# Kernel optimization log

Hardware: AMD Instinct MI355X
Metric: run time of the kernel (lower is better)

The kernel has to match this reference:

```python
import jax, jax.numpy as jnp
import numpy as np

B, N, D, L = 32, 1024, 128, 2  # batch graphs, nodes, hidden dim, num GIN layers
BN_EPS = 1e-5


def _batchnorm(x2d, gamma, beta):
    # Training-mode BatchNorm1d over flattened (B*N, D) with biased variance
    mean = jnp.mean(x2d, axis=0)
    var = jnp.mean(jnp.square(x2d - mean), axis=0)
    return (x2d - mean) * (gamma / jnp.sqrt(var + BN_EPS)) + beta


def setup_inputs() -> dict:
    key = jax.random.key(0)
    ks = jax.random.split(key, 12)
    s = 1.0 / np.sqrt(D)  # torch Linear default init scale
    inp = {
        "x": jax.random.normal(ks[0], (B, N, D), dtype=jnp.float32),
        "padded_nei": jax.random.randint(ks[1], (B, N, 8), 0, N, dtype=jnp.int64),
        "adj": jax.random.uniform(ks[2], (B, N, N), dtype=jnp.float32),
        # stacked per-layer params [L, ...]
        "W1": jax.random.uniform(ks[3], (L, D, D), jnp.float32, -s, s),
        "b1": jax.random.uniform(ks[4], (L, D), jnp.float32, -s, s),
        "W2": jax.random.uniform(ks[5], (L, D, D), jnp.float32, -s, s),
        "b2": jax.random.uniform(ks[6], (L, D), jnp.float32, -s, s),
        "g_in": jnp.ones((L, D), jnp.float32),   # MLP-internal BN gamma
        "be_in": jnp.zeros((L, D), jnp.float32),  # MLP-internal BN beta
        "g_out": jnp.ones((L, D), jnp.float32),  # GraphCNN outer BN gamma
        "be_out": jnp.zeros((L, D), jnp.float32),
    }
    return inp


def reference(x, padded_nei, adj, W1, b1, W2, b2, g_in, be_in, g_out, be_out):
    h = x  # [B, N, D]
    for l in range(L):
        # sum-pooling over neighbors via batched dense adjacency matmul
        pooled = jnp.einsum('bij,bjd->bid', adj, h)  # [B, N, D]
        # MLP: Linear -> BN -> ReLU -> Linear
        z = pooled @ W1[l] + b1[l]
        z = jax.nn.relu(_batchnorm(z.reshape(-1, D), g_in[l], be_in[l])).reshape(B, N, D)
        z = z @ W2[l] + b2[l]
        # outer BatchNorm1d + ReLU
        h = jax.nn.relu(_batchnorm(z.reshape(-1, D), g_out[l], be_out[l])).reshape(B, N, D)
    return h
```

## Files before the change

### kernel.cpp

```cpp
#include <hip/hip_runtime.h>
#include <stdint.h>


#define BB 32
#define NN 1024
#define DD 128
#define RR 32768

typedef __bf16 bf16_t;
typedef bf16_t bf16x8 __attribute__((ext_vector_type(8)));
typedef unsigned short us8 __attribute__((ext_vector_type(8)));
typedef float f32x4 __attribute__((ext_vector_type(4)));

__device__ __forceinline__ unsigned short f2b(float f) {
  unsigned u = __float_as_uint(f);
  u += 0x7fff + ((u >> 16) & 1);
  return (unsigned short)(u >> 16);
}
__device__ __forceinline__ float b2f(unsigned short s) {
  return __uint_as_float((unsigned)s << 16);
}

#define GLL(GP, LP)                                              \
  __builtin_amdgcn_global_load_lds(                              \
      (const __attribute__((address_space(1))) void*)(GP),       \
      (__attribute__((address_space(3))) void*)(LP), 16, 0, 0)

__global__ __launch_bounds__(256) void k0_prep(const float* __restrict__ x,
                                               const float* __restrict__ adj,
                                               const float* __restrict__ W1,
                                               const float* __restrict__ W2,
                                               unsigned short* __restrict__ hT,
                                               unsigned short* __restrict__ W1T,
                                               unsigned short* __restrict__ W2T,
                                               unsigned short* __restrict__ adjB) {
  const int tid = threadIdx.x;
  if (blockIdx.x >= 512) {
    size_t i8 = ((size_t)(blockIdx.x - 512) * 256 + tid) * 8;
    float4 a = *(const float4*)(adj + i8);
    float4 b = *(const float4*)(adj + i8 + 4);
    alignas(16) unsigned short t[8] = {f2b(a.x), f2b(a.y), f2b(a.z), f2b(a.w),
                                       f2b(b.x), f2b(b.y), f2b(b.z), f2b(b.w)};
    *(uint4*)(adjB + i8) = *(const uint4*)t;
    return;
  }
  if (blockIdx.x < 256) {
    const int b = blockIdx.x >> 3, nt = blockIdx.x & 7;
    __shared__ alignas(16) unsigned short T[128][136];
    const int r = tid >> 1, c0 = (tid & 1) * 64;
    const float* src = x + ((size_t)(b * 8 + nt) * 128 + r) * 128 + c0;
#pragma unroll
    for (int i = 0; i < 64; i += 4) {
      float4 v = *(const float4*)(src + i);
      int c = c0 + i;
      T[c][r] = f2b(v.x); T[c + 1][r] = f2b(v.y);
      T[c + 2][r] = f2b(v.z); T[c + 3][r] = f2b(v.w);
    }
    __syncthreads();
    const int d = tid >> 1, n0 = (tid & 1) * 64;
    unsigned short* dst = hT + ((size_t)b * DD + d) * NN + nt * 128 + n0;
#pragma unroll
    for (int i = 0; i < 64; i += 8)
      *(uint4*)(dst + i) = *(const uint4*)&T[d][n0 + i];
  } else {
    int idx = (blockIdx.x - 256) * 256 + tid;
    int w = idx >> 15;
    int rem = idx & 32767;
    int l = rem >> 14;
    int n = (rem >> 7) & 127;
    int k = rem & 127;
    const float* W = w ? W2 : W1;
    unsigned short* WT = w ? W2T : W1T;
    WT[((size_t)l * 128 + n) * 128 + k] = f2b(W[((size_t)l * 128 + k) * 128 + n]);
  }
}

__global__ __launch_bounds__(256, 2) void kA_pool_lin(
    const unsigned short* __restrict__ adjB, const unsigned short* __restrict__ hT,
    const unsigned short* __restrict__ WT, const float* __restrict__ bias,
    unsigned short* __restrict__ z1b, float* __restrict__ gsum,
    float* __restrict__ gsq) {
  const int mt = blockIdx.x, b = blockIdx.y;
  const int tid = threadIdx.x;
  const int wave = tid >> 6, lane = tid & 63;
  const int wc = wave * 32;
  const int ln = lane & 15, q = lane >> 4;

  __shared__ union {
    struct {
      unsigned short A[3][4096];
      unsigned short B[3][8192];
    } s;
    unsigned short As2[64][136];
  } sm;

  bf16x8 wfr[4][2];
#pragma unroll
  for (int ks = 0; ks < 4; ks++)
#pragma unroll
    for (int j = 0; j < 2; j++)
      wfr[ks][j] = *(const bf16x8*)&WT[(size_t)(wc + j * 16 + ln) * 128 + ks * 32 + q * 8];
  asm volatile("s_waitcnt vmcnt(0)" ::: "memory");

  const unsigned short* adjb = adjB + ((size_t)b * NN + mt * 64) * NN;
  const unsigned short* hTb = hT + (size_t)b * DD * NN;

  const int srow = tid >> 3;
  const int sseg = (((tid & 7) ^ (srow & 7)) << 3);
  const unsigned short* gA = adjb + (size_t)srow * NN + sseg;
  const unsigned short* gB = hTb + (size_t)srow * NN + sseg;

#define STAGE(P, K0)                                \
  do {                                              \
    unsigned short* ap = sm.s.A[(P)];               \
    unsigned short* bp = sm.s.B[(P)];               \
    GLL(gA + (K0), ap + tid * 8);                   \
    GLL(gA + 32 * NN + (K0), ap + 2048 + tid * 8);  \
    GLL(gB + (K0), bp + tid * 8);                   \
    GLL(gB + 32 * NN + (K0), bp + 2048 + tid * 8);  \
    GLL(gB + 64 * NN + (K0), bp + 4096 + tid * 8);  \
    GLL(gB + 96 * NN + (K0), bp + 6144 + tid * 8);  \
  } while (0)

  STAGE(0, 0);
  STAGE(1, 64);
  STAGE(2, 128);

  f32x4 acc1[4][2];
  f32x4 zero = {0.f, 0.f, 0.f, 0.f};
#pragma unroll
  for (int i = 0; i < 4; i++) { acc1[i][0] = zero; acc1[i][1] = zero; }

  const int xorv = (ln & 7) << 4;

#pragma unroll
  for (int t = 0; t < 16; ++t) {
    const int p = t % 3;
    if (t < 14)
      asm volatile("s_waitcnt vmcnt(12)" ::: "memory");
    else if (t == 14)
      asm volatile("s_waitcnt vmcnt(6)" ::: "memory");
    else
      asm volatile("s_waitcnt vmcnt(0)" ::: "memory");
    __builtin_amdgcn_s_barrier();
    __builtin_amdgcn_sched_barrier(0);
    {
      const char* Ab = (const char*)sm.s.A[p];
      const char* Bb = (const char*)sm.s.B[p];
#pragma unroll
      for (int kk = 0; kk < 2; kk++) {
        const int co = ((kk << 6) + (q << 4)) ^ xorv;
        bf16x8 af[4], bfr[2];
#pragma unroll
        for (int i = 0; i < 4; i++)
          af[i] = *(const bf16x8*)(Ab + (i * 16 + ln) * 128 + co);
#pragma unroll
        for (int j = 0; j < 2; j++)
          bfr[j] = *(const bf16x8*)(Bb + (wc + j * 16 + ln) * 128 + co);
#pragma unroll
        for (int i = 0; i < 4; i++)
#pragma unroll
          for (int j = 0; j < 2; j++)
            acc1[i][j] = __builtin_amdgcn_mfma_f32_16x16x32_bf16(af[i], bfr[j], acc1[i][j], 0, 0, 0);
      }
    }
    __builtin_amdgcn_sched_barrier(0);
    __builtin_amdgcn_s_barrier();
    __builtin_amdgcn_sched_barrier(0);
    if (t < 13) STAGE(p, (t + 3) * 64);
  }
#undef STAGE

#pragma unroll
  for (int i = 0; i < 4; i++) {
    int row = i * 16 + q * 4;
#pragma unroll
    for (int j = 0; j < 2; j++) {
      int col = wc + j * 16 + ln;
#pragma unroll
      for (int r = 0; r < 4; r++) sm.As2[row + r][col] = f2b(acc1[i][j][r]);
    }
  }
  __syncthreads();

  f32x4 acc2[4][2];
#pragma unroll
  for (int i = 0; i < 4; i++) { acc2[i][0] = zero; acc2[i][1] = zero; }
#pragma unroll
  for (int ks = 0; ks < 4; ks++) {
    bf16x8 af[4];
#pragma unroll
    for (int i = 0; i < 4; i++)
      af[i] = *(const bf16x8*)&sm.As2[i * 16 + ln][ks * 32 + q * 8];
#pragma unroll
    for (int i = 0; i < 4; i++)
#pragma unroll
      for (int j = 0; j < 2; j++)
        acc2[i][j] = __builtin_amdgcn_mfma_f32_16x16x32_bf16(af[i], wfr[ks][j], acc2[i][j], 0, 0, 0);
  }

  const size_t row0 = (size_t)b * NN + mt * 64;
#pragma unroll
  for (int j = 0; j < 2; j++) {
    int col = wc + j * 16 + ln;
    float bc = bias[col];
    float s1 = 0.f, s2 = 0.f;
#pragma unroll
    for (int i = 0; i < 4; i++) {
      int row = i * 16 + q * 4;
#pragma unroll
      for (int r = 0; r < 4; r++) {
        float v = acc2[i][j][r] + bc;
        z1b[(row0 + row + r) * 128 + col] = f2b(v);
        s1 += v; s2 += v * v;
      }
    }
    s1 += __shfl_xor(s1, 16); s1 += __shfl_xor(s1, 32);
    s2 += __shfl_xor(s2, 16); s2 += __shfl_xor(s2, 32);
    if (q == 0) { atomicAdd(&gsum[col], s1); atomicAdd(&gsq[col], s2); }
  }
}

__global__ __launch_bounds__(256, 2) void kB_lin(
    const unsigned short* __restrict__ Zin, const float* __restrict__ gsum_in,
    const float* __restrict__ gsq_in, const float* __restrict__ gamma,
    const float* __restrict__ beta, const unsigned short* __restrict__ WT,
    const float* __restrict__ bias, unsigned short* __restrict__ z2b,
    float* __restrict__ gsum, float* __restrict__ gsq) {
  const int mt = blockIdx.x;
  const int tid = threadIdx.x;
  const int wave = tid >> 6, lane = tid & 63;
  const int wc = wave * 32;
  const int ln = lane & 15, q = lane >> 4;

  __shared__ alignas(16) unsigned short Az[64 * 128];
  __shared__ float nsc[128], nsh[128];

  bf16x8 wfr[4][2];
#pragma unroll
  for (int ks = 0; ks < 4; ks++)
#pragma unroll
    for (int j = 0; j < 2; j++)
      wfr[ks][j] = *(const bf16x8*)&WT[(size_t)(wc + j * 16 + ln) * 128 + ks * 32 + q * 8];

  const size_t row0 = (size_t)mt * 64;
  const int rZ = tid >> 4;
  const int uZ = (((tid & 15) ^ (rZ & 7)) << 3);
  const unsigned short* gZ = Zin + (row0 + rZ) * 128 + uZ;
  GLL(gZ, Az + tid * 8);
  GLL(gZ + 16 * 128, Az + 2048 + tid * 8);
  GLL(gZ + 32 * 128, Az + 4096 + tid * 8);
  GLL(gZ + 48 * 128, Az + 6144 + tid * 8);

  if (tid < 128) {
    float mean = gsum_in[tid] * (1.f / 32768.f);
    float var = gsq_in[tid] * (1.f / 32768.f) - mean * mean;
    float sc = gamma[tid] * rsqrtf(var + 1e-5f);
    nsc[tid] = sc; nsh[tid] = beta[tid] - mean * sc;
  }
  __syncthreads();

  f32x4 acc[4][2];
  f32x4 zero = {0.f, 0.f, 0.f, 0.f};
#pragma unroll
  for (int i = 0; i < 4; i++) { acc[i][0] = zero; acc[i][1] = zero; }

  const int xorv = (ln & 7) << 4;
#pragma unroll
  for (int ks = 0; ks < 4; ks++) {
    bf16x8 af[4];
#pragma unroll
    for (int i = 0; i < 4; i++) {
      us8 raw = *(const us8*)((const char*)Az + (i * 16 + ln) * 256 +
                              (((ks << 6) + (q << 4)) ^ xorv));
      us8 t;
#pragma unroll
      for (int e = 0; e < 8; e++) {
        int col = ks * 32 + q * 8 + e;
        t[e] = f2b(fmaxf(fmaf(b2f(raw[e]), nsc[col], nsh[col]), 0.f));
      }
      af[i] = *(bf16x8*)&t;
    }
#pragma unroll
    for (int i = 0; i < 4; i++)
#pragma unroll
      for (int j = 0; j < 2; j++)
        acc[i][j] = __builtin_amdgcn_mfma_f32_16x16x32_bf16(af[i], wfr[ks][j], acc[i][j], 0, 0, 0);
  }

#pragma unroll
  for (int j = 0; j < 2; j++) {
    int col = wc + j * 16 + ln;
    float bc = bias[col];
    float s1 = 0.f, s2 = 0.f;
#pragma unroll
    for (int i = 0; i < 4; i++) {
      int row = i * 16 + q * 4;
#pragma unroll
      for (int r = 0; r < 4; r++) {
        float v = acc[i][j][r] + bc;
        z2b[(row0 + row + r) * 128 + col] = f2b(v);
        s1 += v; s2 += v * v;
      }
    }
    s1 += __shfl_xor(s1, 16); s1 += __shfl_xor(s1, 32);
    s2 += __shfl_xor(s2, 16); s2 += __shfl_xor(s2, 32);
    if (q == 0) { atomicAdd(&gsum[col], s1); atomicAdd(&gsq[col], s2); }
  }
}

__global__ __launch_bounds__(256) void k4_bnt(const unsigned short* __restrict__ Z,
                                              const float* __restrict__ gsum,
                                              const float* __restrict__ gsq,
                                              const float* __restrict__ gamma,
                                              const float* __restrict__ beta,
                                              unsigned short* __restrict__ hT) {
  const int b = blockIdx.x, nt = blockIdx.y, tid = threadIdx.x;
  __shared__ alignas(16) unsigned short T[128][136];
  __shared__ float nsc[128], nsh[128];
  if (tid < 128) {
    float mean = gsum[tid] * (1.f / 32768.f);
    float var = gsq[tid] * (1.f / 32768.f) - mean * mean;
    float sc = gamma[tid] * rsqrtf(var + 1e-5f);
    nsc[tid] = sc; nsh[tid] = beta[tid] - mean * sc;
  }
  __syncthreads();
  const int r = tid >> 1, c0 = (tid & 1) * 64;
  const unsigned short* src = Z + ((size_t)(b * 8 + nt) * 128 + r) * 128 + c0;
#pragma unroll
  for (int u = 0; u < 8; u++) {
    uint4 raw = *(const uint4*)(src + u * 8);
    const unsigned short* s = (const unsigned short*)&raw;
#pragma unroll
    for (int e = 0; e < 8; e++) {
      int c = c0 + u * 8 + e;
      T[c][r] = f2b(fmaxf(fmaf(b2f(s[e]), nsc[c], nsh[c]), 0.f));
    }
  }
  __syncthreads();
  const int d = tid >> 1, n0 = (tid & 1) * 64;
  unsigned short* dst = hT + ((size_t)b * DD + d) * NN + nt * 128 + n0;
#pragma unroll
  for (int i = 0; i < 64; i += 8)
    *(uint4*)(dst + i) = *(const uint4*)&T[d][n0 + i];
}

__global__ __launch_bounds__(256) void k4_out(const unsigned short* __restrict__ Z,
                                              const float* __restrict__ gsum,
                                              const float* __restrict__ gsq,
                                              const float* __restrict__ gamma,
                                              const float* __restrict__ beta,
                                              float* __restrict__ out) {
  const int blk = blockIdx.x, tid = threadIdx.x;
  __shared__ float nsc[128], nsh[128];
  if (tid < 128) {
    float mean = gsum[tid] * (1.f / 32768.f);
    float var = gsq[tid] * (1.f / 32768.f) - mean * mean;
    float sc = gamma[tid] * rsqrtf(var + 1e-5f);
    nsc[tid] = sc; nsh[tid] = beta[tid] - mean * sc;
  }
  __syncthreads();
  const int r = tid >> 1, c0 = (tid & 1) * 64;
  const unsigned short* src = Z + ((size_t)blk * 128 + r) * 128 + c0;
  float* dst = out + ((size_t)blk * 128 + r) * 128 + c0;
#pragma unroll
  for (int u = 0; u < 8; u++) {
    uint4 raw = *(const uint4*)(src + u * 8);
    const unsigned short* s = (const unsigned short*)&raw;
    float4 o;
    int c = c0 + u * 8;
    o.x = fmaxf(fmaf(b2f(s[0]), nsc[c], nsh[c]), 0.f);
    o.y = fmaxf(fmaf(b2f(s[1]), nsc[c + 1], nsh[c + 1]), 0.f);
    o.z = fmaxf(fmaf(b2f(s[2]), nsc[c + 2], nsh[c + 2]), 0.f);
    o.w = fmaxf(fmaf(b2f(s[3]), nsc[c + 3], nsh[c + 3]), 0.f);
    *(float4*)(dst + u * 8) = o;
    o.x = fmaxf(fmaf(b2f(s[4]), nsc[c + 4], nsh[c + 4]), 0.f);
    o.y = fmaxf(fmaf(b2f(s[5]), nsc[c + 5], nsh[c + 5]), 0.f);
    o.z = fmaxf(fmaf(b2f(s[6]), nsc[c + 6], nsh[c + 6]), 0.f);
    o.w = fmaxf(fmaf(b2f(s[7]), nsc[c + 7], nsh[c + 7]), 0.f);
    *(float4*)(dst + u * 8 + 4) = o;
  }
}

extern "C" void kernel_launch(void* const* d_in, const int* in_sizes, int n_in,
                              void* d_out, int out_size, void* d_ws, size_t ws_size,
                              hipStream_t stream) {
  const float* x = (const float*)d_in[0];
  const float* adj = (const float*)d_in[2];
  const float* W1 = (const float*)d_in[3];
  const float* b1 = (const float*)d_in[4];
  const float* W2 = (const float*)d_in[5];
  const float* b2 = (const float*)d_in[6];
  const float* g_in = (const float*)d_in[7];
  const float* be_in = (const float*)d_in[8];
  const float* g_out = (const float*)d_in[9];
  const float* be_out = (const float*)d_in[10];
  float* out = (float*)d_out;

  char* ws = (char*)d_ws;
  unsigned short* hT = (unsigned short*)ws;
  unsigned short* z1b = (unsigned short*)(ws + 8ull * 1024 * 1024);
  unsigned short* z2b = (unsigned short*)(ws + 16ull * 1024 * 1024);
  unsigned short* W1T = (unsigned short*)(ws + 24ull * 1024 * 1024);
  unsigned short* W2T = W1T + 2 * 128 * 128;
  float* stats = (float*)(ws + 25ull * 1024 * 1024);
  unsigned short* adjB = (unsigned short*)(ws + 26ull * 1024 * 1024);

  hipMemsetAsync(stats, 0, 4 * 256 * sizeof(float), stream);
  k0_prep<<<512 + 16384, 256, 0, stream>>>(x, adj, W1, W2, hT, W1T, W2T, adjB);

  for (int l = 0; l < 2; l++) {
    float* st_in = stats + (l * 2 + 0) * 256;
    float* st_out = stats + (l * 2 + 1) * 256;
    kA_pool_lin<<<dim3(16, 32), 256, 0, stream>>>(adjB, hT, W1T + l * 16384,
                                                  b1 + l * 128, z1b, st_in,
                                                  st_in + 128);
    kB_lin<<<512, 256, 0, stream>>>(z1b, st_in, st_in + 128, g_in + l * 128,
                                    be_in + l * 128, W2T + l * 16384,
                                    b2 + l * 128, z2b, st_out, st_out + 128);
    if (l == 0)
      k4_bnt<<<dim3(32, 8), 256, 0, stream>>>(z2b, st_out, st_out + 128, g_out,
                                              be_out, hT);
    else
      k4_out<<<256, 256, 0, stream>>>(z2b, st_out, st_out + 128, g_out + 128,
                                      be_out + 128, out);
  }
}
```

Before: 350.8 us.

## Load pooling GEMM fragments directly from global into registers with smaller tiles

The pooling GEMM in kA no longer stages adjacency and hT tiles through a triple-buffered LDS pipeline with global_load_lds and barriers. Each wave now loads its MFMA fragments straight from global memory into double-buffered registers, the M tile shrinks from 64 to 32 rows, the grid doubles, and occupancy is raised to 4 blocks per CU. This removes LDS traffic and barrier synchronisation and improves latency hiding through more resident waves. In exchange, data sharing across waves is lost, so adjacency and hT rows are re-read from global/L2 by multiple waves with less coalesced 16-byte per-lane loads.

```diff
diff --git a/kernel.cpp b/kernel.cpp
--- a/kernel.cpp
+++ b/kernel.cpp
@@ -75,7 +75,7 @@
   }
 }
 
-__global__ __launch_bounds__(256, 2) void kA_pool_lin(
+__global__ __launch_bounds__(256, 4) void kA_pool_lin(
     const unsigned short* __restrict__ adjB, const unsigned short* __restrict__ hT,
     const unsigned short* __restrict__ WT, const float* __restrict__ bias,
     unsigned short* __restrict__ z1b, float* __restrict__ gsum,
@@ -86,127 +86,87 @@
   const int wc = wave * 32;
   const int ln = lane & 15, q = lane >> 4;
 
-  __shared__ union {
-    struct {
-      unsigned short A[3][4096];
-      unsigned short B[3][8192];
-    } s;
-    unsigned short As2[64][136];
-  } sm;
-
-  bf16x8 wfr[4][2];
-#pragma unroll
-  for (int ks = 0; ks < 4; ks++)
-#pragma unroll
-    for (int j = 0; j < 2; j++)
-      wfr[ks][j] = *(const bf16x8*)&WT[(size_t)(wc + j * 16 + ln) * 128 + ks * 32 + q * 8];
-  asm volatile("s_waitcnt vmcnt(0)" ::: "memory");
-
-  const unsigned short* adjb = adjB + ((size_t)b * NN + mt * 64) * NN;
-  const unsigned short* hTb = hT + (size_t)b * DD * NN;
-
-  const int srow = tid >> 3;
-  const int sseg = (((tid & 7) ^ (srow & 7)) << 3);
-  const unsigned short* gA = adjb + (size_t)srow * NN + sseg;
-  const unsigned short* gB = hTb + (size_t)srow * NN + sseg;
-
-#define STAGE(P, K0)                                \
-  do {                                              \
-    unsigned short* ap = sm.s.A[(P)];               \
-    unsigned short* bp = sm.s.B[(P)];               \
-    GLL(gA + (K0), ap + tid * 8);                   \
-    GLL(gA + 32 * NN + (K0), ap + 2048 + tid * 8);  \
-    GLL(gB + (K0), bp + tid * 8);                   \
-    GLL(gB + 32 * NN + (K0), bp + 2048 + tid * 8);  \
-    GLL(gB + 64 * NN + (K0), bp + 4096 + tid * 8);  \
-    GLL(gB + 96 * NN + (K0), bp + 6144 + tid * 8);  \
+  __shared__ alignas(16) unsigned short As2[32][136];
+
+  const unsigned short* pA = adjB + ((size_t)b * NN + mt * 32 + ln) * NN + q * 8;
+  const unsigned short* pB = hT + ((size_t)b * DD + wc + ln) * NN + q * 8;
+
+  f32x4 acc1[2][2];
+  f32x4 zero = {0.f, 0.f, 0.f, 0.f};
+#pragma unroll
+  for (int i = 0; i < 2; i++) { acc1[i][0] = zero; acc1[i][1] = zero; }
+
+  bf16x8 fa[2][2][2], fb[2][2][2];
+
+#define LOADC(BUF, K0)                                                        \
+  do {                                                                        \
+    _Pragma("unroll") for (int ii = 0; ii < 2; ii++)                          \
+        _Pragma("unroll") for (int kk = 0; kk < 2; kk++)                      \
+            fa[BUF][ii][kk] =                                                 \
+                *(const bf16x8*)(pA + (size_t)(ii * 16) * NN + (K0) + kk * 32);\
+    _Pragma("unroll") for (int jj = 0; jj < 2; jj++)                          \
+        _Pragma("unroll") for (int kk = 0; kk < 2; kk++)                      \
+            fb[BUF][jj][kk] =                                                 \
+                *(const bf16x8*)(pB + (size_t)(jj * 16) * NN + (K0) + kk * 32);\
   } while (0)
 
-  STAGE(0, 0);
-  STAGE(1, 64);
-  STAGE(2, 128);
-
-  f32x4 acc1[4][2];
-  f32x4 zero = {0.f, 0.f, 0.f, 0.f};
-#pragma unroll
-  for (int i = 0; i < 4; i++) { acc1[i][0] = zero; acc1[i][1] = zero; }
-
-  const int xorv = (ln & 7) << 4;
+  LOADC(0, 0);
+  LOADC(1, 64);
 
 #pragma unroll
   for (int t = 0; t < 16; ++t) {
-    const int p = t % 3;
-    if (t < 14)
-      asm volatile("s_waitcnt vmcnt(12)" ::: "memory");
-    else if (t == 14)
-      asm volatile("s_waitcnt vmcnt(6)" ::: "memory");
-    else
-      asm volatile("s_waitcnt vmcnt(0)" ::: "memory");
-    __builtin_amdgcn_s_barrier();
-    __builtin_amdgcn_sched_barrier(0);
-    {
-      const char* Ab = (const char*)sm.s.A[p];
-      const char* Bb = (const char*)sm.s.B[p];
-#pragma unroll
-      for (int kk = 0; kk < 2; kk++) {
-        const int co = ((kk << 6) + (q << 4)) ^ xorv;
-        bf16x8 af[4], bfr[2];
-#pragma unroll
-        for (int i = 0; i < 4; i++)
-          af[i] = *(const bf16x8*)(Ab + (i * 16 + ln) * 128 + co);
+    const int cur = t & 1;
+#pragma unroll
+    for (int kk = 0; kk < 2; kk++)
+#pragma unroll
+      for (int i = 0; i < 2; i++)
 #pragma unroll
         for (int j = 0; j < 2; j++)
-          bfr[j] = *(const bf16x8*)(Bb + (wc + j * 16 + ln) * 128 + co);
-#pragma unroll
-        for (int i = 0; i < 4; i++)
-#pragma unroll
-          for (int j = 0; j < 2; j++)
-            acc1[i][j] = __builtin_amdgcn_mfma_f32_16x16x32_bf16(af[i], bfr[j], acc1[i][j], 0, 0, 0);
-      }
-    }
-    __builtin_amdgcn_sched_barrier(0);
-    __builtin_amdgcn_s_barrier();
-    __builtin_amdgcn_sched_barrier(0);
-    if (t < 13) STAGE(p, (t + 3) * 64);
-  }
-#undef STAGE
-
-#pragma unroll
-  for (int i = 0; i < 4; i++) {
+          acc1[i][j] = __builtin_amdgcn_mfma_f32_16x16x32_bf16(
+              fa[cur][i][kk], fb[cur][j][kk], acc1[i][j], 0, 0, 0);
+    if (t + 2 < 16) LOADC(cur, (t + 2) * 64);
+  }
+#undef LOADC
+
+#pragma unroll
+  for (int i = 0; i < 2; i++) {
     int row = i * 16 + q * 4;
 #pragma unroll
     for (int j = 0; j < 2; j++) {
       int col = wc + j * 16 + ln;
 #pragma unroll
-      for (int r = 0; r < 4; r++) sm.As2[row + r][col] = f2b(acc1[i][j][r]);
-    }
-  }
-  __syncthreads();
-
-  f32x4 acc2[4][2];
-#pragma unroll
-  for (int i = 0; i < 4; i++) { acc2[i][0] = zero; acc2[i][1] = zero; }
+      for (int r = 0; r < 4; r++) As2[row + r][col] = f2b(acc1[i][j][r]);
+    }
+  }
+  __syncthreads();
+
+  f32x4 acc2[2][2];
+#pragma unroll
+  for (int i = 0; i < 2; i++) { acc2[i][0] = zero; acc2[i][1] = zero; }
 #pragma unroll
   for (int ks = 0; ks < 4; ks++) {
-    bf16x8 af[4];
-#pragma unroll
-    for (int i = 0; i < 4; i++)
-      af[i] = *(const bf16x8*)&sm.As2[i * 16 + ln][ks * 32 + q * 8];
-#pragma unroll
-    for (int i = 0; i < 4; i++)
+    bf16x8 af[2], wf[2];
+#pragma unroll
+    for (int i = 0; i < 2; i++)
+      af[i] = *(const bf16x8*)&As2[i * 16 + ln][ks * 32 + q * 8];
+#pragma unroll
+    for (int j = 0; j < 2; j++)
+      wf[j] = *(const bf16x8*)&WT[(size_t)(wc + j * 16 + ln) * 128 + ks * 32 + q * 8];
+#pragma unroll
+    for (int i = 0; i < 2; i++)
 #pragma unroll
       for (int j = 0; j < 2; j++)
-        acc2[i][j] = __builtin_amdgcn_mfma_f32_16x16x32_bf16(af[i], wfr[ks][j], acc2[i][j], 0, 0, 0);
-  }
-
-  const size_t row0 = (size_t)b * NN + mt * 64;
+        acc2[i][j] = __builtin_amdgcn_mfma_f32_16x16x32_bf16(af[i], wf[j], acc2[i][j], 0, 0, 0);
+  }
+
+  const size_t row0 = (size_t)b * NN + mt * 32;
 #pragma unroll
   for (int j = 0; j < 2; j++) {
     int col = wc + j * 16 + ln;
     float bc = bias[col];
     float s1 = 0.f, s2 = 0.f;
 #pragma unroll
-    for (int i = 0; i < 4; i++) {
+    for (int i = 0; i < 2; i++) {
       int row = i * 16 + q * 4;
 #pragma unroll
       for (int r = 0; r < 4; r++) {
@@ -412,7 +372,7 @@
   for (int l = 0; l < 2; l++) {
     float* st_in = stats + (l * 2 + 0) * 256;
     float* st_out = stats + (l * 2 + 1) * 256;
-    kA_pool_lin<<<dim3(16, 32), 256, 0, stream>>>(adjB, hT, W1T + l * 16384,
+    kA_pool_lin<<<dim3(32, 32), 256, 0, stream>>>(adjB, hT, W1T + l * 16384,
                                                   b1 + l * 128, z1b, st_in,
                                                   st_in + 128);
     kB_lin<<<512, 256, 0, stream>>>(z1b, st_in, st_in + 128, g_in + l * 128,
```

After: 431.3 us. +22.9%, slower.
